# Optimization experiments

Measured on AMD Instinct MI355X. Metric: run time of the kernel, lower is better.

The kernel has to match this reference:

```python
import jax, jax.numpy as jnp
import numpy as np

N_NODES = 50000
N_EDGES = 1000000
HID = 64
L = 3
EPS_MSG = 1e-7   # GENConv message eps
EPS_SM = 1e-16   # PyG scatter-softmax denominator eps
LN_EPS = 1e-5


def layernorm(x, g, b):
    mu = jnp.mean(x, axis=-1, keepdims=True)
    var = jnp.var(x, axis=-1, keepdims=True)
    return (x - mu) * jax.lax.rsqrt(var + LN_EPS) * g + b


def genconv(x, src, dst, edge_attr, t, W1, b1, g1, be1, W2, b2):
    # message: relu(x_j + e_ij) + eps  -> [E, HID]
    msg = jax.nn.relu(x[src] + edge_attr) + EPS_MSG
    # softmax aggregation over incoming edges of each dst node
    logits = msg * t
    m = jax.ops.segment_max(logits, dst, num_segments=N_NODES)
    m = jnp.where(jnp.isfinite(m), m, 0.0)
    e = jnp.exp(logits - m[dst])
    s = jax.ops.segment_sum(e, dst, num_segments=N_NODES) + EPS_SM
    agg = jax.ops.segment_sum((e / s[dst]) * msg, dst, num_segments=N_NODES)
    # root residual + MLP [64 -> 128 -> 64]
    h = agg + x
    h = h @ W1 + b1
    h = jax.nn.relu(layernorm(h, g1, be1))
    return h @ W2 + b2


def setup_inputs() -> dict:
    key = jax.random.key(0)
    ks = jax.random.split(key, 10)
    inp = {
        'x': jax.random.normal(ks[0], (N_NODES, 16), jnp.float32),
        'edge_attr': jax.random.uniform(ks[1], (N_EDGES, 1), jnp.float32),
        'edge_index': jax.random.randint(ks[2], (2, N_EDGES), 0, N_NODES, jnp.int32),
        'W_node': jax.random.normal(ks[3], (16, HID), jnp.float32) / np.sqrt(16.0),
        'b_node': jnp.zeros((HID,), jnp.float32),
        'W_edge': jax.random.normal(ks[4], (1, HID), jnp.float32),
        'b_edge': jnp.zeros((HID,), jnp.float32),
        't': jnp.ones((L,), jnp.float32),
        'W1': jax.random.normal(ks[5], (L, HID, 2 * HID), jnp.float32) / np.sqrt(float(HID)),
        'b1': jnp.zeros((L, 2 * HID), jnp.float32),
        'ln_g': jnp.ones((L, 2 * HID), jnp.float32),
        'ln_b': jnp.zeros((L, 2 * HID), jnp.float32),
        'W2': jax.random.normal(ks[6], (L, 2 * HID, HID), jnp.float32) / np.sqrt(2.0 * HID),
        'b2': jnp.zeros((L, HID), jnp.float32),
        'norm_g': jnp.ones((L, HID), jnp.float32),
        'norm_b': jnp.zeros((L, HID), jnp.float32),
        'W_lin': jax.random.normal(ks[7], (HID, 64), jnp.float32) / np.sqrt(float(HID)),
        'b_lin': jnp.zeros((64,), jnp.float32),
    }
    return inp


def reference(x, edge_attr, edge_index, W_node, b_node, W_edge, b_edge, t,
              W1, b1, ln_g, ln_b, W2, b2, norm_g, norm_b, W_lin, b_lin):
    src, dst = edge_index[0], edge_index[1]
    h = x @ W_node + b_node                 # [N, HID]
    ea = edge_attr @ W_edge + b_edge        # [E, HID]
    # layer 0: conv only
    h = genconv(h, src, dst, ea, t[0], W1[0], b1[0], ln_g[0], ln_b[0], W2[0], b2[0])
    # layers 1..L-1: res+ blocks (norm -> relu -> conv -> residual); dropout is identity in eval
    for i in range(1, L):
        z = jax.nn.relu(layernorm(h, norm_g[i], norm_b[i]))
        h = h + genconv(z, src, dst, ea, t[i], W1[i], b1[i], ln_g[i], ln_b[i], W2[i], b2[i])
    # final norm/act reuses layer 0's norm
    h = jax.nn.relu(layernorm(h, norm_g[0], norm_b[0]))
    # adaptive avg/max pool (N, 64) -> (1, 32): pool over all nodes, channel bins of 2
    avg = h.mean(axis=0).reshape(32, 2).mean(axis=1)
    mx = h.max(axis=0).reshape(32, 2).max(axis=1)
    emb = jnp.concatenate([avg, mx])[None, :]   # [1, 64]
    return emb @ W_lin + b_lin                  # [1, 64]
```

## Files before the change

### kernel.cpp

```cpp
#include <hip/hip_runtime.h>
#include <math.h>

#define N_NODES 50000
#define N_EDGES 1000000
#define HID 64
#define CAP 64
#define N_TILES (N_NODES / 16)
#define NB_MLP 782
#define VB_S 72
#define UB_S 136
#define NB_ENC ((N_NODES + 3) / 4)
#define NB_WPREP ((3 * 8192 + 255) / 256)
#define NBK 196
#define BKCAP 6144
#define EPB 4096
#define NB1 ((N_EDGES + EPB - 1) / EPB)
static_assert(N_NODES % 16 == 0, "tile math");
static_assert(N_NODES <= 65536, "src must fit in 16 bits");

typedef __attribute__((ext_vector_type(8))) short short8;
typedef __attribute__((ext_vector_type(4))) float f32x4;

__device__ __forceinline__ unsigned short f2bf(float x) {
    unsigned u = __float_as_uint(x);
    u += 0x7FFFu + ((u >> 16) & 1u);
    return (unsigned short)(u >> 16);
}
__device__ __forceinline__ float bfbits_hi(unsigned pk) {
    return __uint_as_float(pk & 0xFFFF0000u);
}
__device__ __forceinline__ float bf2f(unsigned short v) {
    return __uint_as_float(((unsigned)v) << 16);
}
__device__ __forceinline__ unsigned addpk(unsigned a, unsigned b) {
    float lo = __uint_as_float(a << 16) + __uint_as_float(b << 16);
    float hi = __uint_as_float(a & 0xFFFF0000u) + __uint_as_float(b & 0xFFFF0000u);
    return (unsigned)f2bf(lo) | ((unsigned)f2bf(hi) << 16);
}

__global__ __launch_bounds__(256) void k_front(
    const float* __restrict__ x, const float* __restrict__ Wn,
    const float* __restrict__ bn, unsigned short* __restrict__ zb,
    const float* __restrict__ W1, const float* __restrict__ W2,
    unsigned short* __restrict__ w1p, unsigned short* __restrict__ w2p,
    const int* __restrict__ ei, const float* __restrict__ eattr,
    int* __restrict__ gcnt, uint2* __restrict__ coarse) {
    __shared__ unsigned pk_l[EPB];
    __shared__ unsigned short dst_l[EPB];
    __shared__ unsigned spk[EPB];
    __shared__ unsigned short sdst[EPB];
    __shared__ int hist[NBK], loc[NBK], gbase[NBK], cur[NBK];
    __shared__ int inc[256];
    int b = blockIdx.x;
    if (b < NB1) {
        int tid = threadIdx.x;
        int e0 = b * EPB;
        int nel = N_EDGES - e0; if (nel > EPB) nel = EPB;
        for (int q = tid; q < NBK; q += 256) { hist[q] = 0; cur[q] = 0; }
        __syncthreads();
        for (int j = tid; j < nel; j += 256) {
            int i = e0 + j;
            int d = ei[N_EDGES + i];
            unsigned pk = ((unsigned)f2bf(eattr[i]) << 16) | (unsigned)(ei[i] & 0xFFFF);
            pk_l[j] = pk; dst_l[j] = (unsigned short)d;
            atomicAdd(&hist[d >> 8], 1);
        }
        __syncthreads();
        int v = (tid < NBK) ? hist[tid] : 0;
        inc[tid] = v;
        __syncthreads();
        #pragma unroll
        for (int dd = 1; dd < 256; dd <<= 1) {
            int t2 = (tid >= dd) ? inc[tid - dd] : 0;
            __syncthreads();
            inc[tid] += t2;
            __syncthreads();
        }
        if (tid < NBK) {
            loc[tid] = inc[tid] - v;
            gbase[tid] = atomicAdd(&gcnt[tid], v);
        }
        __syncthreads();
        for (int j = tid; j < nel; j += 256) {
            int bkt = dst_l[j] >> 8;
            int r = atomicAdd(&cur[bkt], 1);
            int pos = loc[bkt] + r;
            spk[pos] = pk_l[j]; sdst[pos] = dst_l[j];
        }
        __syncthreads();
        for (int j = tid; j < nel; j += 256) {
            int d = sdst[j];
            int bkt = d >> 8;
            int off = gbase[bkt] + (j - loc[bkt]);
            if (off < BKCAP) coarse[(size_t)bkt * BKCAP + off] = make_uint2(spk[j], (unsigned)d);
        }
    } else if (b < NB1 + NB_ENC) {
        int n = (b - NB1) * 4 + (threadIdx.x >> 6);
        int c = threadIdx.x & 63;
        if (n >= N_NODES) return;
        float acc = bn[c];
        const float* xr = x + n * 16;
        #pragma unroll
        for (int k = 0; k < 16; ++k) acc = fmaf(xr[k], Wn[k * 64 + c], acc);
        zb[n * 64 + c] = f2bf(acc);
    } else {
        int i = (b - NB1 - NB_ENC) * 256 + threadIdx.x;
        if (i >= 3 * 8192) return;
        int L = i >> 13, r = i & 8191;
        int j = r & 7, lane = (r >> 3) & 63;
        int quad = lane >> 4, col = lane & 15;
        {
            int st = r >> 9;
            int s = st >> 3, t = st & 7;
            w1p[i] = f2bf(W1[L * 8192 + (s * 32 + quad * 8 + j) * 128 + t * 16 + col]);
        }
        {
            int ft = r >> 9;
            int s = ft >> 2, t = ft & 3;
            w2p[i] = f2bf(W2[L * 8192 + (s * 32 + quad * 8 + j) * 64 + t * 16 + col]);
        }
    }
}

__global__ __launch_bounds__(256) void k_bin2(
    const int* __restrict__ gcnt, const uint2* __restrict__ coarse,
    int* __restrict__ cnt, unsigned int* __restrict__ s_pack) {
    __shared__ unsigned epk[BKCAP];
    __shared__ unsigned char eln[BKCAP];
    __shared__ unsigned spk[BKCAP];
    __shared__ unsigned char sln[BKCAP];
    __shared__ int hist[128], loc[128], cur[128], inc2[128];
    int tid = threadIdx.x;
    int bkt = blockIdx.x >> 1;
    int hsel = blockIdx.x & 1;
    int m = gcnt[bkt]; if (m > BKCAP) m = BKCAP;
    if (tid < 128) { hist[tid] = 0; cur[tid] = 0; }
    __syncthreads();
    for (int j = tid; j < m; j += 256) {
        uint2 e = coarse[(size_t)bkt * BKCAP + j];
        epk[j] = e.x;
        int ln = (int)(e.y & 255u);
        eln[j] = (unsigned char)ln;
        if ((ln >> 7) == hsel) atomicAdd(&hist[ln & 127], 1);
    }
    __syncthreads();
    int v = (tid < 128) ? hist[tid] : 0;
    if (tid < 128) inc2[tid] = v;
    __syncthreads();
    #pragma unroll
    for (int dd = 1; dd < 128; dd <<= 1) {
        int t2 = (tid >= dd && tid < 128) ? inc2[tid - dd] : 0;
        __syncthreads();
        if (tid < 128) inc2[tid] += t2;
        __syncthreads();
    }
    if (tid < 128) {
        loc[tid] = inc2[tid] - v;
        int node = bkt * 256 + hsel * 128 + tid;
        if (node < N_NODES) cnt[node] = v;
    }
    __syncthreads();
    int mh = inc2[127];
    for (int j = tid; j < m; j += 256) {
        int ln = eln[j];
        if ((ln >> 7) == hsel) {
            int r = atomicAdd(&cur[ln & 127], 1);
            int pos = loc[ln & 127] + r;
            spk[pos] = epk[j]; sln[pos] = (unsigned char)ln;
        }
    }
    __syncthreads();
    if (tid < 128 && v > 1) {
        int b0 = loc[tid];
        for (int a = b0 + 1; a < b0 + v; ++a) {
            unsigned key = spk[a];
            int kb = (int)(key & 0xFFFFu);
            int c = a - 1;
            while (c >= b0 && (int)(spk[c] & 0xFFFFu) > kb) {
                spk[c + 1] = spk[c];
                --c;
            }
            spk[c + 1] = key;
        }
    }
    __syncthreads();
    for (int j = tid; j < mh; j += 256) {
        int ln = sln[j];
        int k = j - loc[ln & 127];
        if (k < CAP) s_pack[(size_t)(bkt * 256 + ln) * CAP + k] = spk[j];
    }
}

__global__ __launch_bounds__(256) void k_agg(
    const unsigned short* __restrict__ zb, const int* __restrict__ cnt,
    const unsigned int* __restrict__ s_pack,
    const float* __restrict__ We, const float* __restrict__ be,
    const float* __restrict__ t, int layer, unsigned short* __restrict__ aggb) {
    int wid = (blockIdx.x * blockDim.x + threadIdx.x) >> 6;
    int lane = threadIdx.x & 63;
    if (wid >= N_NODES) return;
    int deg = cnt[wid];
    deg = (deg < CAP) ? deg : CAP;
    int beg = wid * CAP, end = beg + deg;
    int half = lane >> 5;
    int c2 = lane & 31;
    float we0 = We[2 * c2], we1 = We[2 * c2 + 1];
    float bv0 = be[2 * c2], bv1 = be[2 * c2 + 1];
    float tl = t[layer];
    const unsigned* zbu = (const unsigned*)zb;
    float s0 = 0.f, s1 = 0.f, n0 = 0.f, n1 = 0.f;
    int i = beg;
    for (; i + 15 < end; i += 16) {
        unsigned pk[8];
        #pragma unroll
        for (int j = 0; j < 8; ++j) {
            unsigned pa = s_pack[i + 2 * j];
            unsigned pb = s_pack[i + 2 * j + 1];
            pk[j] = half ? pb : pa;
        }
        unsigned zu[8];
        #pragma unroll
        for (int j = 0; j < 8; ++j) zu[j] = zbu[(pk[j] & 0xFFFFu) * 32 + c2];
        #pragma unroll
        for (int j = 0; j < 8; ++j) {
            float ea = bfbits_hi(pk[j]);
            float z0 = __uint_as_float(zu[j] << 16);
            float z1 = __uint_as_float(zu[j] & 0xFFFF0000u);
            float m0 = fmaxf(z0 + fmaf(ea, we0, bv0), 0.f) + 1e-7f;
            float m1 = fmaxf(z1 + fmaf(ea, we1, bv1), 0.f) + 1e-7f;
            float p0 = __expf(m0 * tl), p1 = __expf(m1 * tl);
            s0 += p0; n0 = fmaf(p0, m0, n0);
            s1 += p1; n1 = fmaf(p1, m1, n1);
        }
    }
    for (; i + 7 < end; i += 8) {
        unsigned pk[4];
        #pragma unroll
        for (int j = 0; j < 4; ++j) {
            unsigned pa = s_pack[i + 2 * j];
            unsigned pb = s_pack[i + 2 * j + 1];
            pk[j] = half ? pb : pa;
        }
        unsigned zu[4];
        #pragma unroll
        for (int j = 0; j < 4; ++j) zu[j] = zbu[(pk[j] & 0xFFFFu) * 32 + c2];
        #pragma unroll
        for (int j = 0; j < 4; ++j) {
            float ea = bfbits_hi(pk[j]);
            float z0 = __uint_as_float(zu[j] << 16);
            float z1 = __uint_as_float(zu[j] & 0xFFFF0000u);
            float m0 = fmaxf(z0 + fmaf(ea, we0, bv0), 0.f) + 1e-7f;
            float m1 = fmaxf(z1 + fmaf(ea, we1, bv1), 0.f) + 1e-7f;
            float p0 = __expf(m0 * tl), p1 = __expf(m1 * tl);
            s0 += p0; n0 = fmaf(p0, m0, n0);
            s1 += p1; n1 = fmaf(p1, m1, n1);
        }
    }
    for (; i + 1 < end; i += 2) {
        unsigned pa = s_pack[i], pb = s_pack[i + 1];
        unsigned pk = half ? pb : pa;
        unsigned zu = zbu[(pk & 0xFFFFu) * 32 + c2];
        float ea = bfbits_hi(pk);
        float z0 = __uint_as_float(zu << 16);
        float z1 = __uint_as_float(zu & 0xFFFF0000u);
        float m0 = fmaxf(z0 + fmaf(ea, we0, bv0), 0.f) + 1e-7f;
        float m1 = fmaxf(z1 + fmaf(ea, we1, bv1), 0.f) + 1e-7f;
        float p0 = __expf(m0 * tl), p1 = __expf(m1 * tl);
        s0 += p0; n0 = fmaf(p0, m0, n0);
        s1 += p1; n1 = fmaf(p1, m1, n1);
    }
    if (i < end) {
        unsigned pk = s_pack[i];
        unsigned zu = zbu[(pk & 0xFFFFu) * 32 + c2];
        float ea = bfbits_hi(pk);
        float z0 = __uint_as_float(zu << 16);
        float z1 = __uint_as_float(zu & 0xFFFF0000u);
        float m0 = fmaxf(z0 + fmaf(ea, we0, bv0), 0.f) + 1e-7f;
        float m1 = fmaxf(z1 + fmaf(ea, we1, bv1), 0.f) + 1e-7f;
        float p0 = __expf(m0 * tl), p1 = __expf(m1 * tl);
        if (half == 0) {
            s0 += p0; n0 = fmaf(p0, m0, n0);
            s1 += p1; n1 = fmaf(p1, m1, n1);
        }
    }
    s0 += __shfl_xor(s0, 32, 64); n0 += __shfl_xor(n0, 32, 64);
    s1 += __shfl_xor(s1, 32, 64); n1 += __shfl_xor(n1, 32, 64);
    if (half == 0) {
        unsigned r = (unsigned)f2bf(n0 / (s0 + 1e-16f)) |
                     ((unsigned)f2bf(n1 / (s1 + 1e-16f)) << 16);
        ((unsigned*)aggb)[wid * 32 + c2] = r;
    }
}

__global__ __launch_bounds__(256) void k_mlp(
    const unsigned short* __restrict__ aggb, unsigned short* __restrict__ zb,
    unsigned short* __restrict__ hb,
    const unsigned short* __restrict__ w1p, const unsigned short* __restrict__ w2p,
    const float* __restrict__ b1,
    const float* __restrict__ g1, const float* __restrict__ be1,
    const float* __restrict__ b2,
    const float* __restrict__ ng, const float* __restrict__ nb, int mode,
    float* __restrict__ pb_sum, float* __restrict__ pb_max) {
    __shared__ unsigned short w1s[8192];
    __shared__ unsigned short w2s[8192];
    __shared__ unsigned short vbuf[4][16 * VB_S];
    __shared__ unsigned short ubuf[4][16 * UB_S];
    __shared__ float lssum[4][4][16], lsmax[4][4][16];
    int lane = threadIdx.x & 63;
    int wave = threadIdx.x >> 6;
    int col = lane & 15, quad = lane >> 4;
    unsigned short* vb = vbuf[wave];
    unsigned short* ub = ubuf[wave];

    {
        const uint4* s1 = (const uint4*)w1p;
        const uint4* s2 = (const uint4*)w2p;
        uint4* d1 = (uint4*)w1s;
        uint4* d2 = (uint4*)w2s;
        #pragma unroll
        for (int i = 0; i < 4; ++i) {
            d1[threadIdx.x + i * 256] = s1[threadIdx.x + i * 256];
            d2[threadIdx.x + i * 256] = s2[threadIdx.x + i * 256];
        }
    }
    __syncthreads();

    float b1f[8], g1f[8], e1f[8];
    #pragma unroll
    for (int t = 0; t < 8; ++t) {
        int ch = t * 16 + col;
        b1f[t] = b1[ch]; g1f[t] = g1[ch]; e1f[t] = be1[ch];
    }
    float b2f_[4], ngf[4], nbf[4];
    #pragma unroll
    for (int t = 0; t < 4; ++t) {
        b2f_[t] = b2[t * 16 + col];
        ngf[t] = ng[t * 16 + col];
        nbf[t] = nb[t * 16 + col];
    }

    float psum[4] = {0.f, 0.f, 0.f, 0.f};
    float pmax[4] = {0.f, 0.f, 0.f, 0.f};
    int nd = lane >> 2;
    int cg = (lane & 3) * 16;

    for (int tile = blockIdx.x * 4 + wave; tile < N_TILES; tile += NB_MLP * 4) {
        int n0 = tile * 16;
        const uint4* ap = (const uint4*)(aggb + (size_t)(n0 + nd) * 64 + cg);
        const uint4* zp = (const uint4*)(zb + (size_t)(n0 + nd) * 64 + cg);
        uint4 a0 = ap[0], a1 = ap[1], z0 = zp[0], z1 = zp[1];
        uint4 r0, r1;
        r0.x = addpk(a0.x, z0.x); r0.y = addpk(a0.y, z0.y);
        r0.z = addpk(a0.z, z0.z); r0.w = addpk(a0.w, z0.w);
        r1.x = addpk(a1.x, z1.x); r1.y = addpk(a1.y, z1.y);
        r1.z = addpk(a1.z, z1.z); r1.w = addpk(a1.w, z1.w);
        uint4* vdst = (uint4*)&vb[nd * VB_S + cg];
        vdst[0] = r0;
        vdst[1] = r1;

        short8 af0 = *(const short8*)&vb[col * VB_S + quad * 8];
        short8 af1 = *(const short8*)&vb[col * VB_S + 32 + quad * 8];

        uint4 h0, h1;
        if (mode >= 1) {
            const uint4* hp = (const uint4*)(hb + (size_t)(n0 + nd) * 64 + cg);
            h0 = hp[0]; h1 = hp[1];
        }

        f32x4 au[8];
        #pragma unroll
        for (int t = 0; t < 8; ++t) {
            short8 w0 = *(const short8*)&w1s[((0 * 8 + t) * 64 + lane) * 8];
            short8 w1 = *(const short8*)&w1s[((1 * 8 + t) * 64 + lane) * 8];
            f32x4 c = {0.f, 0.f, 0.f, 0.f};
            c = __builtin_amdgcn_mfma_f32_16x16x32_bf16(af0, w0, c, 0, 0, 0);
            c = __builtin_amdgcn_mfma_f32_16x16x32_bf16(af1, w1, c, 0, 0, 0);
            au[t] = c;
        }
        #pragma unroll
        for (int r = 0; r < 4; ++r) {
            float sx = 0.f, sq = 0.f;
            #pragma unroll
            for (int t = 0; t < 8; ++t) {
                float v = au[t][r] + b1f[t];
                sx += v; sq += v * v;
            }
            #pragma unroll
            for (int mask = 1; mask < 16; mask <<= 1) {
                sx += __shfl_xor(sx, mask, 64);
                sq += __shfl_xor(sq, mask, 64);
            }
            float mu = sx * (1.f / 128.f);
            float var = sq * (1.f / 128.f) - mu * mu;
            float rs = rsqrtf(var + 1e-5f);
            int row = quad * 4 + r;
            #pragma unroll
            for (int t = 0; t < 8; ++t) {
                float v = au[t][r] + b1f[t];
                float y = fmaxf(fmaf((v - mu) * rs, g1f[t], e1f[t]), 0.f);
                ub[row * UB_S + t * 16 + col] = f2bf(y);
            }
        }
        f32x4 oc[4];
        #pragma unroll
        for (int t = 0; t < 4; ++t) oc[t] = (f32x4){0.f, 0.f, 0.f, 0.f};
        #pragma unroll
        for (int s = 0; s < 4; ++s) {
            short8 a = *(const short8*)&ub[col * UB_S + s * 32 + quad * 8];
            #pragma unroll
            for (int t = 0; t < 4; ++t) {
                short8 w = *(const short8*)&w2s[((s * 4 + t) * 64 + lane) * 8];
                oc[t] = __builtin_amdgcn_mfma_f32_16x16x32_bf16(a, w, oc[t], 0, 0, 0);
            }
        }
        if (mode >= 1) {
            uint4* hdst = (uint4*)&vb[nd * VB_S + cg];
            hdst[0] = h0;
            hdst[1] = h1;
        }
        #pragma unroll
        for (int r = 0; r < 4; ++r) {
            int row = quad * 4 + r;
            float val[4];
            #pragma unroll
            for (int t = 0; t < 4; ++t) {
                val[t] = oc[t][r] + b2f_[t];
                if (mode >= 1) val[t] += bf2f(vb[row * VB_S + t * 16 + col]);
            }
            float sx = 0.f, sq = 0.f;
            #pragma unroll
            for (int t = 0; t < 4; ++t) { sx += val[t]; sq += val[t] * val[t]; }
            #pragma unroll
            for (int mask = 1; mask < 16; mask <<= 1) {
                sx += __shfl_xor(sx, mask, 64);
                sq += __shfl_xor(sq, mask, 64);
            }
            float mu = sx * (1.f / 64.f);
            float var = sq * (1.f / 64.f) - mu * mu;
            float rs = rsqrtf(var + 1e-5f);
            #pragma unroll
            for (int t = 0; t < 4; ++t) {
                float y = fmaxf(fmaf((val[t] - mu) * rs, ngf[t], nbf[t]), 0.f);
                if (mode <= 1) {
                    vb[row * VB_S + t * 16 + col] = f2bf(val[t]);
                    ub[row * UB_S + t * 16 + col] = f2bf(y);
                } else {
                    psum[t] += y;
                    pmax[t] = fmaxf(pmax[t], y);
                }
            }
        }
        if (mode <= 1) {
            const uint4* hsrc = (const uint4*)&vb[nd * VB_S + cg];
            const uint4* zsrc = (const uint4*)&ub[nd * UB_S + cg];
            uint4* hdst = (uint4*)(hb + (size_t)(n0 + nd) * 64 + cg);
            uint4* zdst = (uint4*)(zb + (size_t)(n0 + nd) * 64 + cg);
            hdst[0] = hsrc[0]; hdst[1] = hsrc[1];
            zdst[0] = zsrc[0]; zdst[1] = zsrc[1];
        }
    }
    if (mode == 2) {
        #pragma unroll
        for (int t = 0; t < 4; ++t) {
            psum[t] += __shfl_xor(psum[t], 16, 64);
            psum[t] += __shfl_xor(psum[t], 32, 64);
            pmax[t] = fmaxf(pmax[t], __shfl_xor(pmax[t], 16, 64));
            pmax[t] = fmaxf(pmax[t], __shfl_xor(pmax[t], 32, 64));
        }
        if (quad == 0) {
            #pragma unroll
            for (int t = 0; t < 4; ++t) {
                lssum[wave][t][col] = psum[t];
                lsmax[wave][t][col] = pmax[t];
            }
        }
        __syncthreads();
        if (wave == 0) {
            int t = lane >> 4, c = lane & 15;
            float s = lssum[0][t][c] + lssum[1][t][c] + lssum[2][t][c] + lssum[3][t][c];
            float mx = fmaxf(fmaxf(lsmax[0][t][c], lsmax[1][t][c]),
                             fmaxf(lsmax[2][t][c], lsmax[3][t][c]));
            pb_sum[blockIdx.x * 64 + lane] = s;
            pb_max[blockIdx.x * 64 + lane] = mx;
        }
    }
}

__global__ __launch_bounds__(1024) void k_head(
    const float* __restrict__ pb_sum, const float* __restrict__ pb_max,
    const float* __restrict__ Wl, const float* __restrict__ bl, float* __restrict__ out) {
    __shared__ float sa4[16][64], sm4[16][64];
    __shared__ float sa[64], sm[64], emb[64];
    int t = threadIdx.x;
    int ch = t & 63, part = t >> 6;
    float s = 0.f, mx = 0.f;
    for (int b = part; b < NB_MLP; b += 16) {
        s += pb_sum[b * 64 + ch];
        mx = fmaxf(mx, pb_max[b * 64 + ch]);
    }
    sa4[part][ch] = s; sm4[part][ch] = mx;
    __syncthreads();
    if (t < 64) {
        float ss = 0.f, mm = 0.f;
        #pragma unroll
        for (int q = 0; q < 16; ++q) {
            ss += sa4[q][t];
            mm = fmaxf(mm, sm4[q][t]);
        }
        sa[t] = ss; sm[t] = mm;
    }
    __syncthreads();
    if (t < 64) {
        if (t < 32) {
            emb[t] = (sa[2 * t] + sa[2 * t + 1]) * (0.5f / (float)N_NODES);
        } else {
            int i = t - 32;
            emb[t] = fmaxf(sm[2 * i], sm[2 * i + 1]);
        }
    }
    __syncthreads();
    if (t < 64) {
        float acc = bl[t];
        for (int k = 0; k < 64; ++k) acc = fmaf(emb[k], Wl[k * 64 + t], acc);
        out[t] = acc;
    }
}

extern "C" void kernel_launch(void* const* d_in, const int* in_sizes, int n_in,
                              void* d_out, int out_size, void* d_ws, size_t ws_size,
                              hipStream_t stream) {
    const float* x     = (const float*)d_in[0];
    const float* eattr = (const float*)d_in[1];
    const int*   ei    = (const int*)d_in[2];
    const float* Wn    = (const float*)d_in[3];
    const float* bn    = (const float*)d_in[4];
    const float* We    = (const float*)d_in[5];
    const float* be    = (const float*)d_in[6];
    const float* t     = (const float*)d_in[7];
    const float* W1    = (const float*)d_in[8];
    const float* b1    = (const float*)d_in[9];
    const float* lg    = (const float*)d_in[10];
    const float* lb    = (const float*)d_in[11];
    const float* W2    = (const float*)d_in[12];
    const float* b2    = (const float*)d_in[13];
    const float* ng    = (const float*)d_in[14];
    const float* nb    = (const float*)d_in[15];
    const float* Wl    = (const float*)d_in[16];
    const float* bl    = (const float*)d_in[17];
    float* out = (float*)d_out;

    char* p = (char*)d_ws;
    unsigned short* hb = (unsigned short*)p; p += (size_t)N_NODES * 64 * 2;
    unsigned short* zb = (unsigned short*)p; p += (size_t)N_NODES * 64 * 2;
    unsigned short* aggb = (unsigned short*)p; p += (size_t)N_NODES * 64 * 2;
    unsigned int* s_pack = (unsigned int*)p; p += (size_t)N_NODES * CAP * 4;
    int* cnt    = (int*)p;  p += (size_t)N_NODES * 4;
    int* gcnt   = (int*)p;  p += (size_t)256 * 4;
    uint2* coarse = (uint2*)p; p += (size_t)NBK * BKCAP * 8;
    float* pb_sum = (float*)p; p += (size_t)NB_MLP * 64 * 4;
    float* pb_max = (float*)p; p += (size_t)NB_MLP * 64 * 4;
    unsigned short* w1p = (unsigned short*)p; p += (size_t)3 * 8192 * 2;
    unsigned short* w2p = (unsigned short*)p; p += (size_t)3 * 8192 * 2;

    hipMemsetAsync(gcnt, 0, (size_t)NBK * sizeof(int), stream);

    k_front<<<NB1 + NB_ENC + NB_WPREP, 256, 0, stream>>>(
        x, Wn, bn, zb, W1, W2, w1p, w2p, ei, eattr, gcnt, coarse);
    k_bin2<<<NBK * 2, 256, 0, stream>>>(gcnt, coarse, cnt, s_pack);

    k_agg<<<(N_NODES + 3) / 4, 256, 0, stream>>>(zb, cnt, s_pack, We, be, t, 0, aggb);
    k_mlp<<<NB_MLP, 256, 0, stream>>>(aggb, zb, hb, w1p, w2p, b1, lg, lb, b2,
                                      ng + 64, nb + 64, 0, pb_sum, pb_max);
    k_agg<<<(N_NODES + 3) / 4, 256, 0, stream>>>(zb, cnt, s_pack, We, be, t, 1, aggb);
    k_mlp<<<NB_MLP, 256, 0, stream>>>(aggb, zb, hb, w1p + 8192, w2p + 8192,
                                      b1 + 128, lg + 128, lb + 128, b2 + 64,
                                      ng + 128, nb + 128, 1, pb_sum, pb_max);
    k_agg<<<(N_NODES + 3) / 4, 256, 0, stream>>>(zb, cnt, s_pack, We, be, t, 2, aggb);
    k_mlp<<<NB_MLP, 256, 0, stream>>>(aggb, zb, hb, w1p + 2 * 8192, w2p + 2 * 8192,
                                      b1 + 2 * 128, lg + 2 * 128, lb + 2 * 128, b2 + 2 * 64,
                                      ng, nb, 2, pb_sum, pb_max);

    k_head<<<1, 1024, 0, stream>>>(pb_sum, pb_max, Wl, bl, out);
}
```

Baseline: 358.2 us.

## Split node features into channel halves and process four edges per wave in aggregation

Node features are stored as two 32-channel halves (zlo/zhi). Each aggregation block handles one half, and its blocks are interleaved so that same-half blocks run together and the gather working set per half is smaller and more cache friendly. Each wave now processes four edges at once, with 16 lanes per edge, using uint4 loads of the packed edge list and an extra shuffle stage for the reduction. The per-node insertion sort of edges by source is removed, which cuts binning cost but gives up the locality that sorted gathers provided.

Measured after the change: 350.1 us. 1.02x faster.

```diff
diff --git a/kernel.cpp b/kernel.cpp
--- a/kernel.cpp
+++ b/kernel.cpp
@@ -7,6 +7,7 @@
 #define CAP 64
 #define N_TILES (N_NODES / 16)
 #define NB_MLP 782
+#define NB_AGG 25000
 #define VB_S 72
 #define UB_S 136
 #define NB_ENC ((N_NODES + 3) / 4)
@@ -40,7 +41,8 @@
 
 __global__ __launch_bounds__(256) void k_front(
     const float* __restrict__ x, const float* __restrict__ Wn,
-    const float* __restrict__ bn, unsigned short* __restrict__ zb,
+    const float* __restrict__ bn,
+    unsigned short* __restrict__ zlo, unsigned short* __restrict__ zhi,
     const float* __restrict__ W1, const float* __restrict__ W2,
     unsigned short* __restrict__ w1p, unsigned short* __restrict__ w2p,
     const int* __restrict__ ei, const float* __restrict__ eattr,
@@ -102,7 +104,8 @@
         const float* xr = x + n * 16;
         #pragma unroll
         for (int k = 0; k < 16; ++k) acc = fmaf(xr[k], Wn[k * 64 + c], acc);
-        zb[n * 64 + c] = f2bf(acc);
+        if (c < 32) zlo[n * 32 + c] = f2bf(acc);
+        else        zhi[n * 32 + (c - 32)] = f2bf(acc);
     } else {
         int i = (b - NB1 - NB_ENC) * 256 + threadIdx.x;
         if (i >= 3 * 8192) return;
@@ -170,20 +173,6 @@
         }
     }
     __syncthreads();
-    if (tid < 128 && v > 1) {
-        int b0 = loc[tid];
-        for (int a = b0 + 1; a < b0 + v; ++a) {
-            unsigned key = spk[a];
-            int kb = (int)(key & 0xFFFFu);
-            int c = a - 1;
-            while (c >= b0 && (int)(spk[c] & 0xFFFFu) > kb) {
-                spk[c + 1] = spk[c];
-                --c;
-            }
-            spk[c + 1] = key;
-        }
-    }
-    __syncthreads();
     for (int j = tid; j < mh; j += 256) {
         int ln = sln[j];
         int k = j - loc[ln & 127];
@@ -192,40 +181,45 @@
 }
 
 __global__ __launch_bounds__(256) void k_agg(
-    const unsigned short* __restrict__ zb, const int* __restrict__ cnt,
-    const unsigned int* __restrict__ s_pack,
+    const unsigned short* __restrict__ zlo, const unsigned short* __restrict__ zhi,
+    const int* __restrict__ cnt, const unsigned int* __restrict__ s_pack,
     const float* __restrict__ We, const float* __restrict__ be,
-    const float* __restrict__ t, int layer, unsigned short* __restrict__ aggb) {
-    int wid = (blockIdx.x * blockDim.x + threadIdx.x) >> 6;
+    const float* __restrict__ t, int layer, unsigned int* __restrict__ aggb) {
+    int b = blockIdx.x;
+    int r8 = b & 7;
+    int h = (r8 >= 4) ? 1 : 0;
+    int idx = (b >> 3) * 4 + (r8 & 3);
+    int wave = threadIdx.x >> 6;
     int lane = threadIdx.x & 63;
-    if (wid >= N_NODES) return;
-    int deg = cnt[wid];
+    int node = idx * 4 + wave;
+    int e4 = lane >> 4;
+    int c4 = lane & 15;
+    const unsigned* zt = (const unsigned*)(h ? zhi : zlo);
+    int ch = h * 32 + 2 * c4;
+    float we0 = We[ch], we1 = We[ch + 1];
+    float bv0 = be[ch], bv1 = be[ch + 1];
+    float tl = t[layer];
+    int deg = cnt[node];
     deg = (deg < CAP) ? deg : CAP;
-    int beg = wid * CAP, end = beg + deg;
-    int half = lane >> 5;
-    int c2 = lane & 31;
-    float we0 = We[2 * c2], we1 = We[2 * c2 + 1];
-    float bv0 = be[2 * c2], bv1 = be[2 * c2 + 1];
-    float tl = t[layer];
-    const unsigned* zbu = (const unsigned*)zb;
+    int beg = node * CAP, end = beg + deg;
     float s0 = 0.f, s1 = 0.f, n0 = 0.f, n1 = 0.f;
     int i = beg;
     for (; i + 15 < end; i += 16) {
-        unsigned pk[8];
-        #pragma unroll
-        for (int j = 0; j < 8; ++j) {
-            unsigned pa = s_pack[i + 2 * j];
-            unsigned pb = s_pack[i + 2 * j + 1];
-            pk[j] = half ? pb : pa;
-        }
-        unsigned zu[8];
-        #pragma unroll
-        for (int j = 0; j < 8; ++j) zu[j] = zbu[(pk[j] & 0xFFFFu) * 32 + c2];
-        #pragma unroll
-        for (int j = 0; j < 8; ++j) {
-            float ea = bfbits_hi(pk[j]);
-            float z0 = __uint_as_float(zu[j] << 16);
-            float z1 = __uint_as_float(zu[j] & 0xFFFF0000u);
+        uint4 pv[4];
+        #pragma unroll
+        for (int q = 0; q < 4; ++q) pv[q] = *(const uint4*)&s_pack[i + 4 * q];
+        unsigned pk[4];
+        #pragma unroll
+        for (int q = 0; q < 4; ++q)
+            pk[q] = (e4 & 2) ? ((e4 & 1) ? pv[q].w : pv[q].z) : ((e4 & 1) ? pv[q].y : pv[q].x);
+        unsigned zu[4];
+        #pragma unroll
+        for (int q = 0; q < 4; ++q) zu[q] = zt[(pk[q] & 0xFFFFu) * 16 + c4];
+        #pragma unroll
+        for (int q = 0; q < 4; ++q) {
+            float ea = bfbits_hi(pk[q]);
+            float z0 = __uint_as_float(zu[q] << 16);
+            float z1 = __uint_as_float(zu[q] & 0xFFFF0000u);
             float m0 = fmaxf(z0 + fmaf(ea, we0, bv0), 0.f) + 1e-7f;
             float m1 = fmaxf(z1 + fmaf(ea, we1, bv1), 0.f) + 1e-7f;
             float p0 = __expf(m0 * tl), p1 = __expf(m1 * tl);
@@ -233,33 +227,10 @@
             s1 += p1; n1 = fmaf(p1, m1, n1);
         }
     }
-    for (; i + 7 < end; i += 8) {
-        unsigned pk[4];
-        #pragma unroll
-        for (int j = 0; j < 4; ++j) {
-            unsigned pa = s_pack[i + 2 * j];
-            unsigned pb = s_pack[i + 2 * j + 1];
-            pk[j] = half ? pb : pa;
-        }
-        unsigned zu[4];
-        #pragma unroll
-        for (int j = 0; j < 4; ++j) zu[j] = zbu[(pk[j] & 0xFFFFu) * 32 + c2];
-        #pragma unroll
-        for (int j = 0; j < 4; ++j) {
-            float ea = bfbits_hi(pk[j]);
-            float z0 = __uint_as_float(zu[j] << 16);
-            float z1 = __uint_as_float(zu[j] & 0xFFFF0000u);
-            float m0 = fmaxf(z0 + fmaf(ea, we0, bv0), 0.f) + 1e-7f;
-            float m1 = fmaxf(z1 + fmaf(ea, we1, bv1), 0.f) + 1e-7f;
-            float p0 = __expf(m0 * tl), p1 = __expf(m1 * tl);
-            s0 += p0; n0 = fmaf(p0, m0, n0);
-            s1 += p1; n1 = fmaf(p1, m1, n1);
-        }
-    }
-    for (; i + 1 < end; i += 2) {
-        unsigned pa = s_pack[i], pb = s_pack[i + 1];
-        unsigned pk = half ? pb : pa;
-        unsigned zu = zbu[(pk & 0xFFFFu) * 32 + c2];
+    for (; i + 3 < end; i += 4) {
+        uint4 pv = *(const uint4*)&s_pack[i];
+        unsigned pk = (e4 & 2) ? ((e4 & 1) ? pv.w : pv.z) : ((e4 & 1) ? pv.y : pv.x);
+        unsigned zu = zt[(pk & 0xFFFFu) * 16 + c4];
         float ea = bfbits_hi(pk);
         float z0 = __uint_as_float(zu << 16);
         float z1 = __uint_as_float(zu & 0xFFFF0000u);
@@ -270,30 +241,34 @@
         s1 += p1; n1 = fmaf(p1, m1, n1);
     }
     if (i < end) {
-        unsigned pk = s_pack[i];
-        unsigned zu = zbu[(pk & 0xFFFFu) * 32 + c2];
+        int idx2 = i + e4;
+        bool ok = idx2 < end;
+        if (!ok) idx2 = end - 1;
+        unsigned pk = s_pack[idx2];
+        unsigned zu = zt[(pk & 0xFFFFu) * 16 + c4];
         float ea = bfbits_hi(pk);
         float z0 = __uint_as_float(zu << 16);
         float z1 = __uint_as_float(zu & 0xFFFF0000u);
         float m0 = fmaxf(z0 + fmaf(ea, we0, bv0), 0.f) + 1e-7f;
         float m1 = fmaxf(z1 + fmaf(ea, we1, bv1), 0.f) + 1e-7f;
         float p0 = __expf(m0 * tl), p1 = __expf(m1 * tl);
-        if (half == 0) {
-            s0 += p0; n0 = fmaf(p0, m0, n0);
-            s1 += p1; n1 = fmaf(p1, m1, n1);
-        }
-    }
+        s0 += ok ? p0 : 0.f; n0 += ok ? p0 * m0 : 0.f;
+        s1 += ok ? p1 : 0.f; n1 += ok ? p1 * m1 : 0.f;
+    }
+    s0 += __shfl_xor(s0, 16, 64); n0 += __shfl_xor(n0, 16, 64);
+    s1 += __shfl_xor(s1, 16, 64); n1 += __shfl_xor(n1, 16, 64);
     s0 += __shfl_xor(s0, 32, 64); n0 += __shfl_xor(n0, 32, 64);
     s1 += __shfl_xor(s1, 32, 64); n1 += __shfl_xor(n1, 32, 64);
-    if (half == 0) {
+    if (e4 == 0) {
         unsigned r = (unsigned)f2bf(n0 / (s0 + 1e-16f)) |
                      ((unsigned)f2bf(n1 / (s1 + 1e-16f)) << 16);
-        ((unsigned*)aggb)[wid * 32 + c2] = r;
+        aggb[node * 32 + h * 16 + c4] = r;
     }
 }
 
 __global__ __launch_bounds__(256) void k_mlp(
-    const unsigned short* __restrict__ aggb, unsigned short* __restrict__ zb,
+    const unsigned short* __restrict__ aggb,
+    unsigned short* __restrict__ zlo, unsigned short* __restrict__ zhi,
     unsigned short* __restrict__ hb,
     const unsigned short* __restrict__ w1p, const unsigned short* __restrict__ w2p,
     const float* __restrict__ b1,
@@ -343,11 +318,13 @@
     float pmax[4] = {0.f, 0.f, 0.f, 0.f};
     int nd = lane >> 2;
     int cg = (lane & 3) * 16;
+    unsigned short* zhalf = (cg < 32) ? zlo : zhi;
+    int zoff = cg & 31;
 
     for (int tile = blockIdx.x * 4 + wave; tile < N_TILES; tile += NB_MLP * 4) {
         int n0 = tile * 16;
         const uint4* ap = (const uint4*)(aggb + (size_t)(n0 + nd) * 64 + cg);
-        const uint4* zp = (const uint4*)(zb + (size_t)(n0 + nd) * 64 + cg);
+        const uint4* zp = (const uint4*)(zhalf + (size_t)(n0 + nd) * 32 + zoff);
         uint4 a0 = ap[0], a1 = ap[1], z0 = zp[0], z1 = zp[1];
         uint4 r0, r1;
         r0.x = addpk(a0.x, z0.x); r0.y = addpk(a0.y, z0.y);
@@ -454,7 +431,7 @@
             const uint4* hsrc = (const uint4*)&vb[nd * VB_S + cg];
             const uint4* zsrc = (const uint4*)&ub[nd * UB_S + cg];
             uint4* hdst = (uint4*)(hb + (size_t)(n0 + nd) * 64 + cg);
-            uint4* zdst = (uint4*)(zb + (size_t)(n0 + nd) * 64 + cg);
+            uint4* zdst = (uint4*)(zhalf + (size_t)(n0 + nd) * 32 + zoff);
             hdst[0] = hsrc[0]; hdst[1] = hsrc[1];
             zdst[0] = zsrc[0]; zdst[1] = zsrc[1];
         }
@@ -550,8 +527,9 @@
     float* out = (float*)d_out;
 
     char* p = (char*)d_ws;
-    unsigned short* hb = (unsigned short*)p; p += (size_t)N_NODES * 64 * 2;
-    unsigned short* zb = (unsigned short*)p; p += (size_t)N_NODES * 64 * 2;
+    unsigned short* hb  = (unsigned short*)p; p += (size_t)N_NODES * 64 * 2;
+    unsigned short* zlo = (unsigned short*)p; p += (size_t)N_NODES * 32 * 2;
+    unsigned short* zhi = (unsigned short*)p; p += (size_t)N_NODES * 32 * 2;
     unsigned short* aggb = (unsigned short*)p; p += (size_t)N_NODES * 64 * 2;
     unsigned int* s_pack = (unsigned int*)p; p += (size_t)N_NODES * CAP * 4;
     int* cnt    = (int*)p;  p += (size_t)N_NODES * 4;
@@ -565,18 +543,21 @@
     hipMemsetAsync(gcnt, 0, (size_t)NBK * sizeof(int), stream);
 
     k_front<<<NB1 + NB_ENC + NB_WPREP, 256, 0, stream>>>(
-        x, Wn, bn, zb, W1, W2, w1p, w2p, ei, eattr, gcnt, coarse);
+        x, Wn, bn, zlo, zhi, W1, W2, w1p, w2p, ei, eattr, gcnt, coarse);
     k_bin2<<<NBK * 2, 256, 0, stream>>>(gcnt, coarse, cnt, s_pack);
 
-    k_agg<<<(N_NODES + 3) / 4, 256, 0, stream>>>(zb, cnt, s_pack, We, be, t, 0, aggb);
-    k_mlp<<<NB_MLP, 256, 0, stream>>>(aggb, zb, hb, w1p, w2p, b1, lg, lb, b2,
+    k_agg<<<NB_AGG, 256, 0, stream>>>(zlo, zhi, cnt, s_pack, We, be, t, 0,
+                                      (unsigned int*)aggb);
+    k_mlp<<<NB_MLP, 256, 0, stream>>>(aggb, zlo, zhi, hb, w1p, w2p, b1, lg, lb, b2,
                                       ng + 64, nb + 64, 0, pb_sum, pb_max);
-    k_agg<<<(N_NODES + 3) / 4, 256, 0, stream>>>(zb, cnt, s_pack, We, be, t, 1, aggb);
-    k_mlp<<<NB_MLP, 256, 0, stream>>>(aggb, zb, hb, w1p + 8192, w2p + 8192,
+    k_agg<<<NB_AGG, 256, 0, stream>>>(zlo, zhi, cnt, s_pack, We, be, t, 1,
+                                      (unsigned int*)aggb);
+    k_mlp<<<NB_MLP, 256, 0, stream>>>(aggb, zlo, zhi, hb, w1p + 8192, w2p + 8192,
                                       b1 + 128, lg + 128, lb + 128, b2 + 64,
                                       ng + 128, nb + 128, 1, pb_sum, pb_max);
-    k_agg<<<(N_NODES + 3) / 4, 256, 0, stream>>>(zb, cnt, s_pack, We, be, t, 2, aggb);
-    k_mlp<<<NB_MLP, 256, 0, stream>>>(aggb, zb, hb, w1p + 2 * 8192, w2p + 2 * 8192,
+    k_agg<<<NB_AGG, 256, 0, stream>>>(zlo, zhi, cnt, s_pack, We, be, t, 2,
+                                      (unsigned int*)aggb);
+    k_mlp<<<NB_MLP, 256, 0, stream>>>(aggb, zlo, zhi, hb, w1p + 2 * 8192, w2p + 2 * 8192,
                                       b1 + 2 * 128, lg + 2 * 128, lb + 2 * 128, b2 + 2 * 64,
                                       ng, nb, 2, pb_sum, pb_max);
 
```
